# Kernel optimization log

Hardware: AMD Instinct MI355X
Metric: run time of the kernel (lower is better)

The kernel has to match this reference:

```python
import jax, jax.numpy as jnp
import numpy as np

EPS = 1e-5
NUM_GROUPS = 32
NUM_HEADS = 8

def group_norm(x, w, b):
    # x: (B, C, H, W), 32 groups, affine per-channel
    B, C, H, W = x.shape
    xg = x.reshape(B, NUM_GROUPS, C // NUM_GROUPS, H, W)
    mu = xg.mean(axis=(2, 3, 4), keepdims=True)
    var = xg.var(axis=(2, 3, 4), keepdims=True)
    xn = ((xg - mu) * jax.lax.rsqrt(var + EPS)).reshape(B, C, H, W)
    return xn * w[None, :, None, None] + b[None, :, None, None]

def conv1x1(x, w, b):
    # 1x1 conv == per-pixel linear; w: (out, in), x: (B, C, H, W)
    return jnp.einsum('oc,bchw->bohw', w, x) + b[None, :, None, None]

def setup_inputs() -> dict:
    key = jax.random.key(0)
    ks = jax.random.split(key, 4)
    B, C, H, W = 2, 512, 64, 64
    s = 1.0 / np.sqrt(C)
    return {
        'x': jax.random.normal(ks[0], (B, C, H, W), jnp.float32),
        'gn_w': jnp.ones((C,), jnp.float32),
        'gn_b': jnp.zeros((C,), jnp.float32),
        'wq': jax.random.normal(ks[1], (C, C), jnp.float32) * s,
        'bq': jnp.zeros((C,), jnp.float32),
        'wkv': jax.random.normal(ks[2], (2 * C, C), jnp.float32) * s,
        'bkv': jnp.zeros((2 * C,), jnp.float32),
        'wo': jax.random.normal(ks[3], (C, C), jnp.float32) * s,
        'bo': jnp.zeros((C,), jnp.float32),
    }

def reference(x, gn_w, gn_b, wq, bq, wkv, bkv, wo, bo):
    B, C, H, W = x.shape
    hd = C // NUM_HEADS  # head_dim
    residual = x
    x_norm = group_norm(x, gn_w, gn_b)
    q = conv1x1(x_norm, wq, bq).reshape(B, NUM_HEADS, hd, H * W)
    kv = conv1x1(x_norm, wkv, bkv)
    k, v = jnp.split(kv, 2, axis=1)
    k = k.reshape(B, NUM_HEADS, hd, H * W)
    v = v.reshape(B, NUM_HEADS, hd, H * W)
    scale = hd ** (-0.5)
    attn = jnp.einsum('bhdi,bhdj->bhij', q, k) * scale
    attn = jax.nn.softmax(attn, axis=-1)
    out = jnp.einsum('bhij,bhdj->bhdi', attn, v).reshape(B, C, H, W)
    out = conv1x1(out, wo, bo)
    return out + residual
```

## Files before the change

### kernel.cpp

```cpp
#include <hip/hip_runtime.h>
#include <cmath>

typedef __bf16 bf16x8 __attribute__((ext_vector_type(8)));
typedef __bf16 bf16x4 __attribute__((ext_vector_type(4)));
typedef float  f32x4  __attribute__((ext_vector_type(4)));

static __device__ __forceinline__ f32x4 mfma16(bf16x8 a, bf16x8 b, f32x4 c) {
    return __builtin_amdgcn_mfma_f32_16x16x32_bf16(a, b, c, 0, 0, 0);
}

static __device__ __forceinline__ float fast_exp2(float x) {
#if __has_builtin(__builtin_amdgcn_exp2f)
    return __builtin_amdgcn_exp2f(x);
#else
    return exp2f(x);
#endif
}

#define OFF_STATS 0
#define OFF_W     4096
#define OFF_XNT   (OFF_W + 2u*1024*1024)
#define OFF_QKT   (OFF_XNT + 8u*1024*1024)
#define OFF_V     (OFF_QKT + 16u*1024*1024)
#define OFF_OP    (OFF_V + 8u*1024*1024)
#define CHUNK_O   4194304u
#define CHUNK_L   65536u

__global__ __launch_bounds__(256) void cvt_w(const float* __restrict__ wq,
                                             const float* __restrict__ wkv,
                                             const float* __restrict__ wo,
                                             __bf16* __restrict__ dst) {
    int i = blockIdx.x * 256 + threadIdx.x;
    if (i < 262144)      dst[i] = (__bf16)wq[i];
    else if (i < 786432) dst[i] = (__bf16)wkv[i - 262144];
    else                 dst[i] = (__bf16)wo[i - 786432];
}

__global__ __launch_bounds__(256) void gn_stats(const float* __restrict__ x,
                                                float* __restrict__ stats) {
    int blk = blockIdx.x;
    int bg = blk >> 2, chunk = blk & 3;
    const float* base = x + (size_t)bg * 65536 + (size_t)chunk * 16384;
    float s = 0.f, ss = 0.f;
    for (int i = threadIdx.x; i < 4096; i += 256) {
        float4 v = ((const float4*)base)[i];
        s  += v.x + v.y + v.z + v.w;
        ss += v.x*v.x + v.y*v.y + v.z*v.z + v.w*v.w;
    }
    #pragma unroll
    for (int off = 1; off < 64; off <<= 1) {
        s  += __shfl_xor(s,  off);
        ss += __shfl_xor(ss, off);
    }
    __shared__ float red[8];
    int wave = threadIdx.x >> 6;
    if ((threadIdx.x & 63) == 0) { red[wave*2] = s; red[wave*2+1] = ss; }
    __syncthreads();
    if (threadIdx.x == 0) {
        float S  = red[0] + red[2] + red[4] + red[6];
        float SS = red[1] + red[3] + red[5] + red[7];
        atomicAdd(&stats[bg*2],     S);
        atomicAdd(&stats[bg*2 + 1], SS);
    }
}

__global__ __launch_bounds__(256) void gn_apply(const float* __restrict__ x,
                                                const float* __restrict__ stats,
                                                const float* __restrict__ w,
                                                const float* __restrict__ bgn,
                                                __bf16* __restrict__ xnT) {
    int p0 = blockIdx.x * 64, c0 = blockIdx.y * 64, b = blockIdx.z;
    int tid = threadIdx.x, lane = tid & 63, wave = tid >> 6;
    __shared__ float t[64][69];
    #pragma unroll
    for (int i = 0; i < 16; ++i) {
        int cc = i * 4 + wave;
        int c  = c0 + cc;
        int g  = (b << 5) + (c >> 4);
        float mu  = stats[g*2] * (1.f/65536.f);
        float var = stats[g*2+1] * (1.f/65536.f) - mu*mu;
        float rstd = rsqrtf(var + 1e-5f);
        float val = x[((size_t)(b*512 + c) << 12) + p0 + lane];
        t[cc][lane] = (val - mu) * rstd * w[c] + bgn[c];
    }
    __syncthreads();
    #pragma unroll
    for (int i = 0; i < 16; ++i) {
        int pp = i * 4 + wave;
        xnT[((size_t)(b*4096 + p0 + pp) << 9) + c0 + lane] = (__bf16)t[lane][pp];
    }
}

__global__ __launch_bounds__(256) void gemm128_kernel(
    const __bf16* __restrict__ A, const __bf16* __restrict__ B,
    const float* __restrict__ bias, const float* __restrict__ bias2, int nsplit,
    float scale0, void* __restrict__ out,
    int N, int K, long long strideA, long long strideO) {
    const int bz = blockIdx.z;
    A += strideA * bz;
    const int m0 = blockIdx.x * 128, n0 = blockIdx.y * 128;
    const int tid = threadIdx.x, lane = tid & 63, wave = tid >> 6;
    const int quad = lane >> 4, l16 = lane & 15;
    const int wm = (wave >> 1) * 64, wn = (wave & 1) * 64;

    __shared__ __attribute__((aligned(16))) __bf16 lds_a[128][40];
    __shared__ __attribute__((aligned(16))) __bf16 lds_b[128][40];

    f32x4 acc[4][4];
    #pragma unroll
    for (int mt = 0; mt < 4; ++mt)
        #pragma unroll
        for (int nt = 0; nt < 4; ++nt)
            #pragma unroll
            for (int r = 0; r < 4; ++r) acc[mt][nt][r] = 0.f;

    const int row_s = tid >> 2;
    const int kc    = (tid & 3) << 3;

    uint4 ra0, ra1, rb0, rb1;
    const __bf16* Abase = A + (size_t)(m0 + row_s) * K + kc;
    const __bf16* Bbase = B + (size_t)(n0 + row_s) * K + kc;
    ra0 = *(const uint4*)Abase;
    ra1 = *(const uint4*)(Abase + (size_t)64 * K);
    rb0 = *(const uint4*)Bbase;
    rb1 = *(const uint4*)(Bbase + (size_t)64 * K);

    for (int kt = 0; kt < K; kt += 32) {
        *(uint4*)&lds_a[row_s][kc]      = ra0;
        *(uint4*)&lds_a[row_s + 64][kc] = ra1;
        *(uint4*)&lds_b[row_s][kc]      = rb0;
        *(uint4*)&lds_b[row_s + 64][kc] = rb1;
        __syncthreads();
        if (kt + 32 < K) {
            ra0 = *(const uint4*)(Abase + kt + 32);
            ra1 = *(const uint4*)(Abase + kt + 32 + (size_t)64 * K);
            rb0 = *(const uint4*)(Bbase + kt + 32);
            rb1 = *(const uint4*)(Bbase + kt + 32 + (size_t)64 * K);
        }
        bf16x8 af[4], bfr[4];
        #pragma unroll
        for (int mt = 0; mt < 4; ++mt)
            af[mt] = *(const bf16x8*)&lds_a[wm + mt*16 + l16][quad*8];
        #pragma unroll
        for (int nt = 0; nt < 4; ++nt)
            bfr[nt] = *(const bf16x8*)&lds_b[wn + nt*16 + l16][quad*8];
        #pragma unroll
        for (int mt = 0; mt < 4; ++mt)
            #pragma unroll
            for (int nt = 0; nt < 4; ++nt)
                acc[mt][nt] = mfma16(af[mt], bfr[nt], acc[mt][nt]);
        __syncthreads();
    }

    #pragma unroll
    for (int mt = 0; mt < 4; ++mt) {
        const int mrow = m0 + wm + mt*16 + quad*4;
        #pragma unroll
        for (int nt = 0; nt < 4; ++nt) {
            const int ncol = n0 + wn + nt*16 + l16;
            #pragma unroll
            for (int r = 0; r < 4; ++r) {
                const int m = mrow + r;
                float bval = (ncol < nsplit) ? bias[ncol] : bias2[ncol - nsplit];
                float val = acc[mt][nt][r] + bval;
                if (ncol < nsplit) val *= scale0;
                ((__bf16*)out)[(size_t)strideO * bz + (size_t)m * N + ncol] = (__bf16)val;
            }
        }
    }
}

template<int OUT_F32, int HAS_RES>
__global__ __launch_bounds__(256) void gemm64_kernel(
    const __bf16* __restrict__ A, const __bf16* __restrict__ B,
    const float* __restrict__ bias, const float* __restrict__ res,
    void* __restrict__ out,
    int N, int K, long long strideB, long long strideO) {
    const int bz = blockIdx.z;
    B += strideB * bz;
    const int m0 = blockIdx.x * 64, n0 = blockIdx.y * 128;
    const int tid = threadIdx.x, lane = tid & 63, wave = tid >> 6;
    const int quad = lane >> 4, l16 = lane & 15;
    const int wn = wave * 32;

    __shared__ __attribute__((aligned(16))) __bf16 lds_a[64][40];
    __shared__ __attribute__((aligned(16))) __bf16 lds_b[128][40];

    f32x4 acc[4][2];
    #pragma unroll
    for (int mt = 0; mt < 4; ++mt)
        #pragma unroll
        for (int nt = 0; nt < 2; ++nt)
            #pragma unroll
            for (int r = 0; r < 4; ++r) acc[mt][nt][r] = 0.f;

    const int row_s = tid >> 2;
    const int kc    = (tid & 3) << 3;

    uint4 ra0, rb0, rb1;
    const __bf16* Abase = A + (size_t)(m0 + row_s) * K + kc;
    const __bf16* Bbase = B + (size_t)(n0 + row_s) * K + kc;
    ra0 = *(const uint4*)Abase;
    rb0 = *(const uint4*)Bbase;
    rb1 = *(const uint4*)(Bbase + (size_t)64 * K);

    for (int kt = 0; kt < K; kt += 32) {
        *(uint4*)&lds_a[row_s][kc]      = ra0;
        *(uint4*)&lds_b[row_s][kc]      = rb0;
        *(uint4*)&lds_b[row_s + 64][kc] = rb1;
        __syncthreads();
        if (kt + 32 < K) {
            ra0 = *(const uint4*)(Abase + kt + 32);
            rb0 = *(const uint4*)(Bbase + kt + 32);
            rb1 = *(const uint4*)(Bbase + kt + 32 + (size_t)64 * K);
        }
        bf16x8 af[4], bfr[2];
        #pragma unroll
        for (int mt = 0; mt < 4; ++mt)
            af[mt] = *(const bf16x8*)&lds_a[mt*16 + l16][quad*8];
        #pragma unroll
        for (int nt = 0; nt < 2; ++nt)
            bfr[nt] = *(const bf16x8*)&lds_b[wn + nt*16 + l16][quad*8];
        #pragma unroll
        for (int mt = 0; mt < 4; ++mt)
            #pragma unroll
            for (int nt = 0; nt < 2; ++nt)
                acc[mt][nt] = mfma16(af[mt], bfr[nt], acc[mt][nt]);
        __syncthreads();
    }

    #pragma unroll
    for (int mt = 0; mt < 4; ++mt) {
        const int mrow = m0 + mt*16 + quad*4;
        #pragma unroll
        for (int nt = 0; nt < 2; ++nt) {
            const int ncol = n0 + wn + nt*16 + l16;
            #pragma unroll
            for (int r = 0; r < 4; ++r) {
                const int m = mrow + r;
                float val = acc[mt][nt][r] + bias[m];
                const size_t idx = (size_t)strideO * bz + (size_t)m * N + ncol;
                if constexpr (HAS_RES) val += res[idx];
                if constexpr (OUT_F32) ((float*)out)[idx] = val;
                else ((__bf16*)out)[idx] = (__bf16)val;
            }
        }
    }
}

template<int NCH>
__global__ __launch_bounds__(256, 3) void attn_kernel(const __bf16* __restrict__ qkT,
                                                      const __bf16* __restrict__ v,
                                                      __bf16* __restrict__ attnT,
                                                      __bf16* __restrict__ Opart,
                                                      float* __restrict__ Lpart) {
    const int b = blockIdx.y >> 3, h = blockIdx.y & 7;
    const int chunk = (NCH > 1) ? blockIdx.z : 0;
    const int NITER = 64 / NCH;
    const int kt0 = chunk * (4096 / NCH);
    const int tid = threadIdx.x;
    const int wave = tid >> 6, lane = tid & 63;
    const int quad = lane >> 4, l16 = lane & 15;
    const int qbase = blockIdx.x * 256 + wave * 64;

    const __bf16* qkTb = qkT + ((size_t)b << 22);
    const __bf16* vb   = v   + ((size_t)b << 21);

    __shared__ __attribute__((aligned(16))) __bf16 lds_k[64][64];
    __shared__ __attribute__((aligned(16))) __bf16 lds_v[80][64];
    __shared__ __attribute__((aligned(16))) __bf16 lds_p[4][64][68];

    bf16x8 aq[4][2];
    #pragma unroll
    for (int mt = 0; mt < 4; ++mt) {
        const __bf16* qrow = qkTb + (size_t)(qbase + mt*16 + l16) * 1024 + h*64 + quad*8;
        aq[mt][0] = *(const bf16x8*)qrow;
        aq[mt][1] = *(const bf16x8*)(qrow + 32);
    }
    f32x4 o[4][5];
    #pragma unroll
    for (int mt = 0; mt < 4; ++mt)
        #pragma unroll
        for (int dt = 0; dt < 5; ++dt)
            #pragma unroll
            for (int r = 0; r < 4; ++r) o[mt][dt][r] = 0.f;
    const f32x4 kZero = {0.f, 0.f, 0.f, 0.f};

    const int srow = tid >> 2;
    const int sc   = tid & 3;
    const int sw0  = ( sc      ^ (srow & 7)) * 8;
    const int sw1  = ((sc + 4) ^ (srow & 7)) * 8;

    const __bf16* kg0 = qkTb + (size_t)srow * 1024 + 512 + h*64 + sc*8;
    const __bf16* vg0 = vb + ((size_t)(h*64 + srow) << 12) + sc*8;

    if (tid < 64) lds_v[64][tid] = (__bf16)1.0f;

    uint4 ck0, ck1, cv0, cv1;
    {
        const __bf16* kg = kg0 + (size_t)kt0 * 1024;
        const __bf16* vg = vg0 + kt0;
        ck0 = *(const uint4*)kg; ck1 = *(const uint4*)(kg + 32);
        cv0 = *(const uint4*)vg; cv1 = *(const uint4*)(vg + 32);
    }

    for (int it = 0; it < NITER; ++it) {
        *(uint4*)&lds_k[srow][sw0] = ck0;
        *(uint4*)&lds_k[srow][sw1] = ck1;
        *(uint4*)&lds_v[srow][sw0] = cv0;
        *(uint4*)&lds_v[srow][sw1] = cv1;
        __syncthreads();
        if (it + 1 < NITER) {
            const int kt = kt0 + (it + 1) * 64;
            const __bf16* kg = kg0 + (size_t)kt * 1024;
            const __bf16* vg = vg0 + kt;
            ck0 = *(const uint4*)kg; ck1 = *(const uint4*)(kg + 32);
            cv0 = *(const uint4*)vg; cv1 = *(const uint4*)(vg + 32);
        }

        #pragma unroll
        for (int nt = 0; nt < 4; ++nt) {
            const int kr = nt*16 + l16;
            bf16x8 bk0 = *(const bf16x8*)&lds_k[kr][( quad      ^ (l16 & 7)) * 8];
            bf16x8 bk1 = *(const bf16x8*)&lds_k[kr][((4 + quad) ^ (l16 & 7)) * 8];
            #pragma unroll
            for (int mt = 0; mt < 4; ++mt) {
                f32x4 s = mfma16(bk1, aq[mt][1], mfma16(bk0, aq[mt][0], kZero));
                f32x4 p;
                #pragma unroll
                for (int r = 0; r < 4; ++r) p[r] = fast_exp2(s[r]);
                bf16x4 pb = __builtin_convertvector(p, bf16x4);
                *(bf16x4*)&lds_p[wave][mt*16 + l16][nt*16 + quad*4] = pb;
            }
        }

        #pragma unroll
        for (int kc = 0; kc < 2; ++kc) {
            bf16x8 pa[4];
            #pragma unroll
            for (int mt = 0; mt < 4; ++mt) {
                bf16x4 plo = *(const bf16x4*)&lds_p[wave][mt*16 + l16][kc*32 + quad*8];
                bf16x4 phi = *(const bf16x4*)&lds_p[wave][mt*16 + l16][kc*32 + quad*8 + 4];
                pa[mt] = __builtin_shufflevector(plo, phi, 0, 1, 2, 3, 4, 5, 6, 7);
            }
            #pragma unroll
            for (int dt = 0; dt < 5; ++dt) {
                bf16x8 bv = *(const bf16x8*)&lds_v[dt*16 + l16][((kc*4 + quad) ^ (l16 & 7)) * 8];
                #pragma unroll
                for (int mt = 0; mt < 4; ++mt)
                    o[mt][dt] = mfma16(pa[mt], bv, o[mt][dt]);
            }
        }
        __syncthreads();
    }

    if constexpr (NCH > 1) {
        __bf16* Ob = Opart + (size_t)chunk * CHUNK_O;
        #pragma unroll
        for (int mt = 0; mt < 4; ++mt)
            #pragma unroll
            for (int dt = 0; dt < 4; ++dt)
                #pragma unroll
                for (int r = 0; r < 4; ++r) {
                    size_t row = (size_t)b * 4096 + qbase + mt*16 + quad*4 + r;
                    Ob[(row << 9) + (h << 6) + dt*16 + l16] = (__bf16)o[mt][dt][r];
                }
        if (l16 == 0) {
            #pragma unroll
            for (int mt = 0; mt < 4; ++mt)
                #pragma unroll
                for (int r = 0; r < 4; ++r) {
                    int p = qbase + mt*16 + quad*4 + r;
                    Lpart[(size_t)chunk * CHUNK_L + (size_t)(((b*8 + h)) << 12) + p] = o[mt][4][r];
                }
        }
    } else {
        #pragma unroll
        for (int mt = 0; mt < 4; ++mt) {
            float inv[4];
            #pragma unroll
            for (int r = 0; r < 4; ++r)
                inv[r] = 1.f / __shfl(o[mt][4][r], lane & 48);
            #pragma unroll
            for (int dt = 0; dt < 4; ++dt)
                #pragma unroll
                for (int r = 0; r < 4; ++r) {
                    size_t row = (size_t)b * 4096 + qbase + mt*16 + quad*4 + r;
                    attnT[(row << 9) + (h << 6) + dt*16 + l16] = (__bf16)(o[mt][dt][r] * inv[r]);
                }
        }
    }
}

template<int NCH>
__global__ __launch_bounds__(256) void attn_combine(const __bf16* __restrict__ Opart,
                                                    const float* __restrict__ Lpart,
                                                    __bf16* __restrict__ attnT) {
    int i = blockIdx.x * 256 + threadIdx.x;
    int c4 = i & 127;
    int p  = (i >> 7) & 4095;
    int b  = i >> 19;
    int h  = c4 >> 4;
    size_t lidx = (size_t)((b*8 + h) << 12) + p;
    float l = 0.f;
    #pragma unroll
    for (int ch = 0; ch < NCH; ++ch) l += Lpart[(size_t)ch * CHUNK_L + lidx];
    float inv = 1.f / l;
    size_t oi = ((size_t)(b*4096 + p) << 9) + c4*4;
    float acc[4] = {0.f, 0.f, 0.f, 0.f};
    #pragma unroll
    for (int ch = 0; ch < NCH; ++ch) {
        bf16x4 ov = *(const bf16x4*)&Opart[(size_t)ch * CHUNK_O + oi];
        #pragma unroll
        for (int r = 0; r < 4; ++r) acc[r] += (float)ov[r];
    }
    bf16x4 rv;
    #pragma unroll
    for (int r = 0; r < 4; ++r) rv[r] = (__bf16)(acc[r] * inv);
    *(bf16x4*)&attnT[oi] = rv;
}

extern "C" void kernel_launch(void* const* d_in, const int* in_sizes, int n_in,
                              void* d_out, int out_size, void* d_ws, size_t ws_size,
                              hipStream_t stream) {
    const float* x   = (const float*)d_in[0];
    const float* gnw = (const float*)d_in[1];
    const float* gnb = (const float*)d_in[2];
    const float* wq  = (const float*)d_in[3];
    const float* bq  = (const float*)d_in[4];
    const float* wkv = (const float*)d_in[5];
    const float* bkv = (const float*)d_in[6];
    const float* wo  = (const float*)d_in[7];
    const float* bo  = (const float*)d_in[8];
    float* out = (float*)d_out;

    char* ws = (char*)d_ws;
    float*  stats  = (float*)(ws + OFF_STATS);
    __bf16* wbf    = (__bf16*)(ws + OFF_W);
    __bf16* wkv_bf = wbf + 262144;
    __bf16* wo_bf  = wbf + 786432;
    __bf16* xnT    = (__bf16*)(ws + OFF_XNT);
    __bf16* qkT    = (__bf16*)(ws + OFF_QKT);
    __bf16* vv     = (__bf16*)(ws + OFF_V);
    __bf16* Opart  = (__bf16*)(ws + OFF_OP);
    __bf16* attnT  = xnT;

    const size_t need4 = (size_t)OFF_OP + 4u * (CHUNK_O * 2 + CHUNK_L * 4);
    const size_t need2 = (size_t)OFF_OP + 2u * (CHUNK_O * 2 + CHUNK_L * 4);
    const int nch = (ws_size >= need4) ? 4 : (ws_size >= need2 ? 2 : 1);
    float* Lpart = (float*)(ws + OFF_OP + (size_t)nch * CHUNK_O * 2);

    hipMemsetAsync(stats, 0, 512, stream);
    cvt_w<<<4096, 256, 0, stream>>>(wq, wkv, wo, wbf);
    gn_stats<<<256, 256, 0, stream>>>(x, stats);
    gn_apply<<<dim3(64, 8, 2), 256, 0, stream>>>(x, stats, gnw, gnb, xnT);

    const long long S = 2097152LL;
    const long long S2 = 4194304LL;
    gemm128_kernel<<<dim3(32, 8, 2), 256, 0, stream>>>(
        xnT, wbf, bq, bkv, 512, 0.125f * 1.44269504f, qkT, 1024, 512, S, S2);
    gemm64_kernel<0,0><<<dim3(8, 32, 2), 256, 0, stream>>>(
        wkv_bf + 262144, xnT, bkv + 512, nullptr, vv, 4096, 512, S, S);

    if (nch == 4) {
        attn_kernel<4><<<dim3(16, 16, 4), 256, 0, stream>>>(qkT, vv, nullptr, Opart, Lpart);
        attn_combine<4><<<4096, 256, 0, stream>>>(Opart, Lpart, attnT);
    } else if (nch == 2) {
        attn_kernel<2><<<dim3(16, 16, 2), 256, 0, stream>>>(qkT, vv, nullptr, Opart, Lpart);
        attn_combine<2><<<4096, 256, 0, stream>>>(Opart, Lpart, attnT);
    } else {
        attn_kernel<1><<<dim3(16, 16, 1), 256, 0, stream>>>(qkT, vv, attnT, nullptr, nullptr);
    }

    gemm64_kernel<1,1><<<dim3(8, 32, 2), 256, 0, stream>>>(
        wo_bf, attnT, bo, x, out, 4096, 512, S, S);
}
```

Baseline: 225.5 us.

## Double-buffer K/V via direct global-to-LDS loads and keep P in registers

Staging of K and V tiles now uses global_load_lds directly into double-buffered LDS, replacing the register round trip and letting one barrier per iteration cover the buffer swap. The P tile is no longer written to and re-read from LDS. It is rearranged in registers with permlane32/permlane16 swaps into the A-operand layout for the PV MFMA. The ones row is replaced by a constant register vector for the row-sum MFMA. This removes LDS traffic and a barrier but relies on gfx950 permlane swap instructions and the exact lane mapping being correct.

```diff
diff --git a/kernel.cpp b/kernel.cpp
--- a/kernel.cpp
+++ b/kernel.cpp
@@ -4,6 +4,7 @@
 typedef __bf16 bf16x8 __attribute__((ext_vector_type(8)));
 typedef __bf16 bf16x4 __attribute__((ext_vector_type(4)));
 typedef float  f32x4  __attribute__((ext_vector_type(4)));
+typedef unsigned uint2_ev __attribute__((ext_vector_type(2)));
 
 static __device__ __forceinline__ f32x4 mfma16(bf16x8 a, bf16x8 b, f32x4 c) {
     return __builtin_amdgcn_mfma_f32_16x16x32_bf16(a, b, c, 0, 0, 0);
@@ -15,6 +16,23 @@
 #else
     return exp2f(x);
 #endif
+}
+
+static __device__ __forceinline__ void quad_swap(unsigned &a, unsigned &b) {
+#if __has_builtin(__builtin_amdgcn_permlane32_swap) && __has_builtin(__builtin_amdgcn_permlane16_swap)
+    uint2_ev r32 = __builtin_amdgcn_permlane32_swap(a, b, false, false);
+    uint2_ev r16 = __builtin_amdgcn_permlane16_swap(r32[0], r32[1], false, false);
+    a = r16[0]; b = r16[1];
+#else
+    asm volatile("v_permlane32_swap_b32 %0, %1\n\t"
+                 "v_permlane16_swap_b32 %0, %1"
+                 : "+v"(a), "+v"(b));
+#endif
+}
+
+static __device__ __forceinline__ void gload_lds16(const void* g, void* l) {
+    __builtin_amdgcn_global_load_lds((const __attribute__((address_space(1))) void*)g,
+                                     (__attribute__((address_space(3))) void*)l, 16, 0, 0);
 }
 
 #define OFF_STATS 0
@@ -266,9 +284,8 @@
     const __bf16* qkTb = qkT + ((size_t)b << 22);
     const __bf16* vb   = v   + ((size_t)b << 21);
 
-    __shared__ __attribute__((aligned(16))) __bf16 lds_k[64][64];
-    __shared__ __attribute__((aligned(16))) __bf16 lds_v[80][64];
-    __shared__ __attribute__((aligned(16))) __bf16 lds_p[4][64][68];
+    __shared__ __attribute__((aligned(16))) __bf16 lds_k[2][64][64];
+    __shared__ __attribute__((aligned(16))) __bf16 lds_v[2][64][64];
 
     bf16x8 aq[4][2];
     #pragma unroll
@@ -286,72 +303,76 @@
             for (int r = 0; r < 4; ++r) o[mt][dt][r] = 0.f;
     const f32x4 kZero = {0.f, 0.f, 0.f, 0.f};
 
-    const int srow = tid >> 2;
-    const int sc   = tid & 3;
-    const int sw0  = ( sc      ^ (srow & 7)) * 8;
-    const int sw1  = ((sc + 4) ^ (srow & 7)) * 8;
-
-    const __bf16* kg0 = qkTb + (size_t)srow * 1024 + 512 + h*64 + sc*8;
-    const __bf16* vg0 = vb + ((size_t)(h*64 + srow) << 12) + sc*8;
-
-    if (tid < 64) lds_v[64][tid] = (__bf16)1.0f;
-
-    uint4 ck0, ck1, cv0, cv1;
-    {
-        const __bf16* kg = kg0 + (size_t)kt0 * 1024;
-        const __bf16* vg = vg0 + kt0;
-        ck0 = *(const uint4*)kg; ck1 = *(const uint4*)(kg + 32);
-        cv0 = *(const uint4*)vg; cv1 = *(const uint4*)(vg + 32);
-    }
+    bf16x8 onesb;
+    #pragma unroll
+    for (int e = 0; e < 8; ++e) onesb[e] = (__bf16)1.0f;
+
+    const int myrow = (wave << 3) + (lane >> 3);
+    const int mych  = ((lane & 7) ^ (myrow & 7)) << 3;
+    const __bf16* kgb = qkTb + (size_t)myrow * 1024 + 512 + h*64 + mych;
+    const __bf16* vgb = vb + ((size_t)(h*64 + myrow) << 12) + mych;
+
+    auto stage = [&](int buf, int kt) {
+        char* kb = (char*)(&lds_k[buf][0][0]) + (wave << 10);
+        char* vp = (char*)(&lds_v[buf][0][0]) + (wave << 10);
+        const __bf16* kg = kgb + (size_t)kt * 1024;
+        const __bf16* vg = vgb + kt;
+        gload_lds16(kg,                       kb);
+        gload_lds16(kg + 32*1024,             kb + 4096);
+        gload_lds16(vg,                       vp);
+        gload_lds16(vg + ((size_t)32 << 12),  vp + 4096);
+    };
+
+    stage(0, kt0);
 
     for (int it = 0; it < NITER; ++it) {
-        *(uint4*)&lds_k[srow][sw0] = ck0;
-        *(uint4*)&lds_k[srow][sw1] = ck1;
-        *(uint4*)&lds_v[srow][sw0] = cv0;
-        *(uint4*)&lds_v[srow][sw1] = cv1;
         __syncthreads();
-        if (it + 1 < NITER) {
-            const int kt = kt0 + (it + 1) * 64;
-            const __bf16* kg = kg0 + (size_t)kt * 1024;
-            const __bf16* vg = vg0 + kt;
-            ck0 = *(const uint4*)kg; ck1 = *(const uint4*)(kg + 32);
-            cv0 = *(const uint4*)vg; cv1 = *(const uint4*)(vg + 32);
-        }
-
-        #pragma unroll
-        for (int nt = 0; nt < 4; ++nt) {
-            const int kr = nt*16 + l16;
-            bf16x8 bk0 = *(const bf16x8*)&lds_k[kr][( quad      ^ (l16 & 7)) * 8];
-            bf16x8 bk1 = *(const bf16x8*)&lds_k[kr][((4 + quad) ^ (l16 & 7)) * 8];
+        const int cur = it & 1;
+        if (it + 1 < NITER) stage(cur ^ 1, kt0 + (it + 1) * 64);
+
+        #pragma unroll
+        for (int kh = 0; kh < 2; ++kh) {
+            unsigned pd[4][4];
+            #pragma unroll
+            for (int j = 0; j < 2; ++j) {
+                const int nt = kh*2 + j;
+                const int kr = nt*16 + l16;
+                bf16x8 bk0 = *(const bf16x8*)&lds_k[cur][kr][( quad      ^ (l16 & 7)) * 8];
+                bf16x8 bk1 = *(const bf16x8*)&lds_k[cur][kr][((4 + quad) ^ (l16 & 7)) * 8];
+                #pragma unroll
+                for (int mt = 0; mt < 4; ++mt) {
+                    f32x4 s = mfma16(bk1, aq[mt][1], mfma16(bk0, aq[mt][0], kZero));
+                    f32x4 p;
+                    #pragma unroll
+                    for (int r = 0; r < 4; ++r) p[r] = fast_exp2(s[r]);
+                    bf16x4 pb = __builtin_convertvector(p, bf16x4);
+                    union { bf16x4 v; unsigned d[2]; } u; u.v = pb;
+                    pd[mt][j*2]     = u.d[0];
+                    pd[mt][j*2 + 1] = u.d[1];
+                }
+            }
+            bf16x8 pa[4];
             #pragma unroll
             for (int mt = 0; mt < 4; ++mt) {
-                f32x4 s = mfma16(bk1, aq[mt][1], mfma16(bk0, aq[mt][0], kZero));
-                f32x4 p;
-                #pragma unroll
-                for (int r = 0; r < 4; ++r) p[r] = fast_exp2(s[r]);
-                bf16x4 pb = __builtin_convertvector(p, bf16x4);
-                *(bf16x4*)&lds_p[wave][mt*16 + l16][nt*16 + quad*4] = pb;
+                unsigned x0 = pd[mt][0], x1 = pd[mt][1];
+                unsigned y0 = pd[mt][2], y1 = pd[mt][3];
+                quad_swap(x0, y0);
+                quad_swap(x1, y1);
+                union { unsigned d[4]; bf16x8 v; } u;
+                u.d[0] = x0; u.d[1] = x1; u.d[2] = y0; u.d[3] = y1;
+                pa[mt] = u.v;
             }
-        }
-
-        #pragma unroll
-        for (int kc = 0; kc < 2; ++kc) {
-            bf16x8 pa[4];
-            #pragma unroll
-            for (int mt = 0; mt < 4; ++mt) {
-                bf16x4 plo = *(const bf16x4*)&lds_p[wave][mt*16 + l16][kc*32 + quad*8];
-                bf16x4 phi = *(const bf16x4*)&lds_p[wave][mt*16 + l16][kc*32 + quad*8 + 4];
-                pa[mt] = __builtin_shufflevector(plo, phi, 0, 1, 2, 3, 4, 5, 6, 7);
-            }
-            #pragma unroll
-            for (int dt = 0; dt < 5; ++dt) {
-                bf16x8 bv = *(const bf16x8*)&lds_v[dt*16 + l16][((kc*4 + quad) ^ (l16 & 7)) * 8];
+            #pragma unroll
+            for (int dt = 0; dt < 4; ++dt) {
+                bf16x8 bv = *(const bf16x8*)&lds_v[cur][dt*16 + l16][((kh*4 + quad) ^ (l16 & 7)) * 8];
                 #pragma unroll
                 for (int mt = 0; mt < 4; ++mt)
                     o[mt][dt] = mfma16(pa[mt], bv, o[mt][dt]);
             }
-        }
-        __syncthreads();
+            #pragma unroll
+            for (int mt = 0; mt < 4; ++mt)
+                o[mt][4] = mfma16(pa[mt], onesb, o[mt][4]);
+        }
     }
 
     if constexpr (NCH > 1) {
```

Result: no change. 223.3 us (-1.0%).
